# Kernel optimization log

Measured on AMD Instinct MI355X. Metric: run time of the kernel, lower is better.

## Reference

```python
import jax, jax.numpy as jnp
import numpy as np

N_MID = 100000
D = 64
B = 64
S = 256
K = 10
BIG_NEG = -2.0**32 + 1.0


def _din(q, facts, mask, W1, b1, W2, b2, W3, b3):
    # q broadcastable to facts shape; facts [..., T, D]; mask [..., T]
    qb = jnp.broadcast_to(q, facts.shape)
    x = jnp.concatenate([qb, facts, qb - facts, qb * facts], axis=-1)  # [..., T, 4D]
    h = jax.nn.sigmoid(x @ W1 + b1)
    h = jax.nn.sigmoid(h @ W2 + b2)
    s = (h @ W3 + b3)[..., 0]  # [..., T]
    s = jnp.where(mask == 1.0, s, BIG_NEG)
    a = jax.nn.softmax(s, axis=-1)
    return jnp.einsum('...t,...td->...d', a, facts)


def _prelu(x, alpha):
    return jnp.maximum(x, 0.0) + alpha * jnp.minimum(x, 0.0)


def setup_inputs():
    key = jax.random.key(0)
    ks = iter(jax.random.split(key, 48))
    def nrm(shape, scale=0.05):
        return jax.random.normal(next(ks), shape, dtype=jnp.float32) * scale
    inp = {}
    inp['mid'] = jax.random.randint(next(ks), (B,), 0, N_MID)
    inp['click_his'] = jax.random.randint(next(ks), (B, S), 0, N_MID)
    inp['unclick_his'] = jax.random.randint(next(ks), (B, K * S), 0, N_MID)
    inp['click_mask'] = jnp.ones((B, S), jnp.float32)
    inp['unclick_mask'] = jnp.ones((B, K * S), jnp.float32)
    inp['emb'] = nrm((N_MID, D), 0.1)
    for p in ('s', 'c', 'u'):  # search / click / unclick attention MLPs
        inp[p + 'W1'] = nrm((4 * D, 80)); inp[p + 'b1'] = jnp.zeros((80,), jnp.float32)
        inp[p + 'W2'] = nrm((80, 40));    inp[p + 'b2'] = jnp.zeros((40,), jnp.float32)
        inp[p + 'W3'] = nrm((40, 1));     inp[p + 'b3'] = jnp.zeros((1,), jnp.float32)
    F = 3 * D
    inp['bn_g'] = jnp.ones((F,), jnp.float32); inp['bn_b'] = jnp.zeros((F,), jnp.float32)
    inp['bn_m'] = jnp.zeros((F,), jnp.float32); inp['bn_v'] = jnp.ones((F,), jnp.float32)
    inp['fW1'] = nrm((F, 200)); inp['fb1'] = jnp.zeros((200,), jnp.float32); inp['a1'] = 0.25 * jnp.ones((200,), jnp.float32)
    inp['fW2'] = nrm((200, 80)); inp['fb2'] = jnp.zeros((80,), jnp.float32); inp['a2'] = 0.25 * jnp.ones((80,), jnp.float32)
    inp['fW3'] = nrm((80, 2)); inp['fb3'] = jnp.zeros((2,), jnp.float32)
    return inp


def reference(mid, click_his, unclick_his, click_mask, unclick_mask, emb,
              sW1, sb1, sW2, sb2, sW3, sb3,
              cW1, cb1, cW2, cb2, cW3, cb3,
              uW1, ub1, uW2, ub2, uW3, ub3,
              bn_g, bn_b, bn_m, bn_v,
              fW1, fb1, a1, fW2, fb2, a2, fW3, fb3):
    item = emb[mid]                                        # [B, D]
    click = emb[click_his] * click_mask[..., None]         # [B, S, D]
    unclick = emb[unclick_his] * unclick_mask[..., None]   # [B, K*S, D]
    uf = unclick.reshape(B, S, K, D)
    umask = unclick_mask.reshape(B, S, K)
    # din_attention_1: per clicked item, attend over its K unclicked items
    un_att = _din(click[:, :, None, :], uf, umask, sW1, sb1, sW2, sb2, sW3, sb3)  # [B, S, D]
    # denoise: project unclick rep onto click rep (shared component)
    dot = jnp.sum(un_att * click, axis=-1, keepdims=True)
    nrm2 = jnp.sum(click * click, axis=-1, keepdims=True) + 1e-12  # ||target||^2
    shared = dot * click / nrm2
    att1 = _din(item[:, None, :], click + shared, click_mask, cW1, cb1, cW2, cb2, cW3, cb3)  # [B, D]
    att2 = _din(item[:, None, :], un_att, click_mask, uW1, ub1, uW2, ub2, uW3, ub3)          # [B, D]
    x = jnp.concatenate([item, att1, att2], axis=-1)  # [B, 3D]
    x = (x - bn_m) / jnp.sqrt(bn_v + 1e-3) * bn_g + bn_b  # inference batchnorm
    x = _prelu(x @ fW1 + fb1, a1)
    x = _prelu(x @ fW2 + fb2, a2)
    logits = x @ fW3 + fb3
    return jax.nn.softmax(logits, axis=-1) + 1e-8
```

## Files before the change

kernel.cpp:

```cpp
#include <hip/hip_runtime.h>
#include <hip/hip_bf16.h>
#include <math.h>

#define BB 64
#define SS 256
#define KK 10
#define DD 64
#define FF 192
#define FH1 200
#define FH2 80
#define BIG_NEG_F (-4294967295.0f)

#define XSTR 200
#define H1STR 104

#define W1ELTS (80 * XSTR)
#define W2ELTS (48 * H1STR)
#define WREG   (W1ELTS + W2ELTS)

typedef __bf16 bfrag __attribute__((ext_vector_type(8)));
typedef float f32x4 __attribute__((ext_vector_type(4)));

__device__ __forceinline__ float sigm_(float x) { return 1.0f / (1.0f + __expf(-x)); }

__global__ __launch_bounds__(256) void k_prep(
    const float* __restrict__ sW1, const float* __restrict__ sW2,
    const float* __restrict__ cW1, const float* __restrict__ cW2,
    const float* __restrict__ uW1, const float* __restrict__ uW2,
    __bf16* __restrict__ Wt)
{
    const int p = blockIdx.x, g = blockIdx.y;
    const float* W1 = (p == 0) ? sW1 : (p == 1) ? cW1 : uW1;
    const float* W2 = (p == 0) ? sW2 : (p == 1) ? cW2 : uW2;
    __bf16* o1 = Wt + p * WREG;
    __bf16* o2 = o1 + W1ELTS;
    for (int e = g * 256 + threadIdx.x; e < W1ELTS; e += 2560) {
        const int n = e / XSTR, k = e % XSTR;
        float v = 0.0f;
        if (k < 64)       v = W1[k * 80 + n] + W1[(128 + k) * 80 + n];
        else if (k < 128) { const int kk = k - 64;  v = W1[(64 + kk) * 80 + n] - W1[(128 + kk) * 80 + n]; }
        else if (k < 192) { const int kk = k - 128; v = W1[(192 + kk) * 80 + n]; }
        o1[e] = (__bf16)v;
    }
    for (int e = g * 256 + threadIdx.x; e < W2ELTS; e += 2560) {
        const int n = e / H1STR, k = e % H1STR;
        o2[e] = (__bf16)((n < 40 && k < 80) ? W2[k * 40 + n] : 0.0f);
    }
}

__device__ __forceinline__ void mlp_core(
    const float* qv, const float* fv,
    const __bf16* __restrict__ sW1, __bf16* __restrict__ sH1w,
    const bfrag* wb2, const float* b1v, const float* b2v, const float* w3v,
    int quad, int l15, float* score)
{
    bfrag af[6];
    #pragma unroll
    for (int j = 0; j < 8; ++j) {
        af[0][j] = (__bf16)qv[j];
        af[1][j] = (__bf16)qv[8 + j];
        af[2][j] = (__bf16)fv[j];
        af[3][j] = (__bf16)fv[8 + j];
        af[4][j] = (__bf16)(qv[j] * fv[j]);
        af[5][j] = (__bf16)(qv[8 + j] * fv[8 + j]);
    }

    f32x4 acc[5];
    #pragma unroll
    for (int nt = 0; nt < 5; ++nt) acc[nt] = (f32x4){0.f, 0.f, 0.f, 0.f};
    {
        const __bf16* wbase = sW1 + l15 * XSTR + quad * 8;
        #pragma unroll
        for (int nt = 0; nt < 5; ++nt) {
            const __bf16* wp = wbase + nt * 16 * XSTR;
            #pragma unroll
            for (int kc = 0; kc < 6; ++kc)
                acc[nt] = __builtin_amdgcn_mfma_f32_16x16x32_bf16(
                    af[kc], *(const bfrag*)(wp + kc * 32), acc[nt], 0, 0, 0);
        }
    }

    #pragma unroll
    for (int nt = 0; nt < 5; ++nt) {
        #pragma unroll
        for (int rg = 0; rg < 4; ++rg)
            sH1w[(quad * 4 + rg) * H1STR + nt * 16 + l15] =
                (__bf16)sigm_(acc[nt][rg] + b1v[nt]);
    }
    #pragma unroll
    for (int rg = 0; rg < 4; ++rg)
        sH1w[(quad * 4 + rg) * H1STR + 80 + l15] = (__bf16)0.0f;

    bfrag af2[3];
    {
        const __bf16* hrow = sH1w + l15 * H1STR + quad * 8;
        #pragma unroll
        for (int kc = 0; kc < 3; ++kc) af2[kc] = *(const bfrag*)(hrow + kc * 32);
    }
    f32x4 acc2[3];
    #pragma unroll
    for (int nt = 0; nt < 3; ++nt) acc2[nt] = (f32x4){0.f, 0.f, 0.f, 0.f};
    #pragma unroll
    for (int nt = 0; nt < 3; ++nt)
        #pragma unroll
        for (int kc = 0; kc < 3; ++kc)
            acc2[nt] = __builtin_amdgcn_mfma_f32_16x16x32_bf16(
                af2[kc], wb2[nt * 3 + kc], acc2[nt], 0, 0, 0);

    float part[4] = {0.f, 0.f, 0.f, 0.f};
    #pragma unroll
    for (int nt = 0; nt < 3; ++nt) {
        #pragma unroll
        for (int rg = 0; rg < 4; ++rg)
            part[rg] += sigm_(acc2[nt][rg] + b2v[nt]) * w3v[nt];
    }
    #pragma unroll
    for (int off = 1; off < 16; off <<= 1) {
        #pragma unroll
        for (int rg = 0; rg < 4; ++rg)
            part[rg] += __shfl_xor(part[rg], off, 64);
    }
    #pragma unroll
    for (int rg = 0; rg < 4; ++rg) score[rg] = part[rg];
}

__global__ __launch_bounds__(320) void k_din0(
    const int* __restrict__ click_his, const int* __restrict__ unclick_his,
    const float* __restrict__ click_mask, const float* __restrict__ unclick_mask,
    const float* __restrict__ emb, const __bf16* __restrict__ Wt,
    const float* __restrict__ b1, const float* __restrict__ b2,
    const float* __restrict__ W3, const float* __restrict__ b3,
    float* __restrict__ unatt, float* __restrict__ coef)
{
    __shared__ __align__(16) __bf16 sW1[80 * XSTR];
    __shared__ __align__(16) __bf16 sH1[5 * 16 * H1STR];
    __shared__ float ssc[80];

    const int t = threadIdx.x;
    const int wave = t >> 6, lane = t & 63;
    const int quad = lane >> 4, l15 = lane & 15;

    {
        const uint4* s1 = (const uint4*)Wt;
        uint4* d1 = (uint4*)sW1;
        for (int e = t; e < W1ELTS / 8; e += 320) d1[e] = s1[e];
    }

    bfrag wb2[9];
    float b1v[5], b2v[3], w3v[3];
    {
        const __bf16* w2g = Wt + W1ELTS;
        #pragma unroll
        for (int nt = 0; nt < 3; ++nt)
            #pragma unroll
            for (int kc = 0; kc < 3; ++kc)
                wb2[nt * 3 + kc] = *(const bfrag*)(w2g + (nt * 16 + l15) * H1STR + kc * 32 + quad * 8);
        #pragma unroll
        for (int nt = 0; nt < 5; ++nt) b1v[nt] = b1[nt * 16 + l15];
        #pragma unroll
        for (int nt = 0; nt < 3; ++nt) {
            const int n = nt * 16 + l15;
            b2v[nt] = (n < 40) ? b2[n] : 0.0f;
            w3v[nt] = (n < 40) ? W3[n] : 0.0f;
        }
    }
    const float b3v = b3[0];

    const int row = 16 * wave + l15;
    const int m   = blockIdx.x * 80 + row;
    const int bs  = blockIdx.x * 8 + row / 10;
    float qv[16], fv[16];
    {
        const float* qp = emb + (size_t)click_his[bs] * DD;
        const float* fp = emb + (size_t)unclick_his[m] * DD;
        const float qs = click_mask[bs], fs = unclick_mask[m];
        const int c = quad * 8;
        *(float4*)(qv + 0)  = *(const float4*)(qp + c);
        *(float4*)(qv + 4)  = *(const float4*)(qp + c + 4);
        *(float4*)(qv + 8)  = *(const float4*)(qp + 32 + c);
        *(float4*)(qv + 12) = *(const float4*)(qp + 32 + c + 4);
        *(float4*)(fv + 0)  = *(const float4*)(fp + c);
        *(float4*)(fv + 4)  = *(const float4*)(fp + c + 4);
        *(float4*)(fv + 8)  = *(const float4*)(fp + 32 + c);
        *(float4*)(fv + 12) = *(const float4*)(fp + 32 + c + 4);
        #pragma unroll
        for (int i = 0; i < 16; ++i) { qv[i] *= qs; fv[i] *= fs; }
    }
    __syncthreads();

    float score[4];
    mlp_core(qv, fv, sW1, sH1 + wave * 16 * H1STR, wb2, b1v, b2v, w3v, quad, l15, score);

    if (l15 == 0) {
        #pragma unroll
        for (int rg = 0; rg < 4; ++rg) {
            const int r2 = 16 * wave + quad * 4 + rg;
            const int m2 = blockIdx.x * 80 + r2;
            ssc[r2] = (unclick_mask[m2] == 1.0f) ? (score[rg] + b3v) : BIG_NEG_F;
        }
    }
    __syncthreads();

    for (int j = wave; j < 8; j += 5) {
        const int bsj = blockIdx.x * 8 + j;
        float a[KK];
        float mx = -INFINITY;
        #pragma unroll
        for (int k = 0; k < KK; ++k) { a[k] = ssc[j * KK + k]; mx = fmaxf(mx, a[k]); }
        float sum = 0.0f;
        #pragma unroll
        for (int k = 0; k < KK; ++k) { a[k] = __expf(a[k] - mx); sum += a[k]; }
        const float inv = 1.0f / sum;
        float acc3 = 0.0f;
        #pragma unroll
        for (int k = 0; k < KK; ++k) {
            const int off = bsj * KK + k;
            acc3 += a[k] * (emb[(size_t)unclick_his[off] * DD + lane] * unclick_mask[off]);
        }
        acc3 *= inv;
        unatt[(size_t)bsj * DD + lane] = acc3;
        const float qv2 = emb[(size_t)click_his[bsj] * DD + lane] * click_mask[bsj];
        float dp = acc3 * qv2, nq = qv2 * qv2;
        #pragma unroll
        for (int o = 32; o > 0; o >>= 1) {
            dp += __shfl_down(dp, o, 64);
            nq += __shfl_down(nq, o, 64);
        }
        if (lane == 0) coef[bsj] = 1.0f + dp / (nq + 1e-12f);
    }
}

__global__ __launch_bounds__(256) void k_din12(
    const int* __restrict__ mid, const int* __restrict__ click_his,
    const float* __restrict__ click_mask,
    const float* __restrict__ emb, const float* __restrict__ unatt,
    const float* __restrict__ coef, const __bf16* __restrict__ Wt,
    const float* __restrict__ cb1, const float* __restrict__ cb2,
    const float* __restrict__ cW3, const float* __restrict__ cb3,
    const float* __restrict__ ub1, const float* __restrict__ ub2,
    const float* __restrict__ uW3, const float* __restrict__ ub3,
    float* __restrict__ scores_c, float* __restrict__ scores_u)
{
    __shared__ __align__(16) __bf16 sW1[80 * XSTR];
    __shared__ __align__(16) __bf16 sH1[4 * 16 * H1STR];

    const int t = threadIdx.x;
    const int mode = blockIdx.y;
    const int wave = t >> 6, lane = t & 63;
    const int quad = lane >> 4, l15 = lane & 15;

    const float* b1 = mode ? ub1 : cb1;
    const float* b2 = mode ? ub2 : cb2;
    const float* W3 = mode ? uW3 : cW3;
    const float* b3 = mode ? ub3 : cb3;
    const __bf16* wreg = Wt + (mode + 1) * WREG;

    {
        const uint4* s1 = (const uint4*)wreg;
        uint4* d1 = (uint4*)sW1;
        for (int e = t; e < W1ELTS / 8; e += 256) d1[e] = s1[e];
    }

    bfrag wb2[9];
    float b1v[5], b2v[3], w3v[3];
    {
        const __bf16* w2g = wreg + W1ELTS;
        #pragma unroll
        for (int nt = 0; nt < 3; ++nt)
            #pragma unroll
            for (int kc = 0; kc < 3; ++kc)
                wb2[nt * 3 + kc] = *(const bfrag*)(w2g + (nt * 16 + l15) * H1STR + kc * 32 + quad * 8);
        #pragma unroll
        for (int nt = 0; nt < 5; ++nt) b1v[nt] = b1[nt * 16 + l15];
        #pragma unroll
        for (int nt = 0; nt < 3; ++nt) {
            const int n = nt * 16 + l15;
            b2v[nt] = (n < 40) ? b2[n] : 0.0f;
            w3v[nt] = (n < 40) ? W3[n] : 0.0f;
        }
    }
    const float b3v = b3[0];

    const int row = 16 * wave + l15;
    const int m   = blockIdx.x * 64 + row;
    const int b   = m >> 8;
    float qv[16], fv[16];
    {
        const float* qp = emb + (size_t)mid[b] * DD;
        const float* fp; float fs;
        if (mode == 0) { fp = emb + (size_t)click_his[m] * DD; fs = click_mask[m] * coef[m]; }
        else           { fp = unatt + (size_t)m * DD; fs = 1.0f; }
        const int c = quad * 8;
        *(float4*)(qv + 0)  = *(const float4*)(qp + c);
        *(float4*)(qv + 4)  = *(const float4*)(qp + c + 4);
        *(float4*)(qv + 8)  = *(const float4*)(qp + 32 + c);
        *(float4*)(qv + 12) = *(const float4*)(qp + 32 + c + 4);
        *(float4*)(fv + 0)  = *(const float4*)(fp + c);
        *(float4*)(fv + 4)  = *(const float4*)(fp + c + 4);
        *(float4*)(fv + 8)  = *(const float4*)(fp + 32 + c);
        *(float4*)(fv + 12) = *(const float4*)(fp + 32 + c + 4);
        #pragma unroll
        for (int i = 0; i < 16; ++i) fv[i] *= fs;
    }
    __syncthreads();

    float score[4];
    mlp_core(qv, fv, sW1, sH1 + wave * 16 * H1STR, wb2, b1v, b2v, w3v, quad, l15, score);

    if (l15 == 0) {
        float* dst = mode ? scores_u : scores_c;
        #pragma unroll
        for (int rg = 0; rg < 4; ++rg) {
            const int m2 = blockIdx.x * 64 + 16 * wave + quad * 4 + rg;
            dst[m2] = (click_mask[m2] == 1.0f) ? (score[rg] + b3v) : BIG_NEG_F;
        }
    }
}

__global__ __launch_bounds__(256) void k_tail(
    const int* __restrict__ mid, const int* __restrict__ click_his,
    const float* __restrict__ click_mask,
    const float* __restrict__ emb, const float* __restrict__ unatt,
    const float* __restrict__ coef,
    const float* __restrict__ scores_c, const float* __restrict__ scores_u,
    const float* __restrict__ bn_g, const float* __restrict__ bn_b,
    const float* __restrict__ bn_m, const float* __restrict__ bn_v,
    const float* __restrict__ fW1, const float* __restrict__ fb1, const float* __restrict__ a1,
    const float* __restrict__ fW2, const float* __restrict__ fb2, const float* __restrict__ a2,
    const float* __restrict__ fW3, const float* __restrict__ fb3,
    float* __restrict__ out)
{
    const int b = blockIdx.x, t = threadIdx.x;
    const int lane = t & 63, wv = t >> 6;

    __shared__ float x[FF];
    __shared__ float sa[SS];
    __shared__ float red[8];
    __shared__ float part[4][DD];
    __shared__ float h1[FH1];
    __shared__ float h2[FH2];

    if (t < DD) x[t] = emb[(size_t)mid[b] * DD + t];

    for (int ty = 0; ty < 2; ++ty) {
        const float sc = (ty ? scores_u : scores_c)[b * SS + t];
        float m = sc;
        #pragma unroll
        for (int o = 32; o > 0; o >>= 1) m = fmaxf(m, __shfl_down(m, o, 64));
        if (lane == 0) red[wv] = m;
        __syncthreads();
        m = fmaxf(fmaxf(red[0], red[1]), fmaxf(red[2], red[3]));
        const float e = __expf(sc - m);
        sa[t] = e;
        float s = e;
        #pragma unroll
        for (int o = 32; o > 0; o >>= 1) s += __shfl_down(s, o, 64);
        if (lane == 0) red[4 + wv] = s;
        __syncthreads();
        const float inv = 1.0f / (red[4] + red[5] + red[6] + red[7]);

        float acc = 0.0f;
        for (int s2 = wv * 64; s2 < wv * 64 + 64; ++s2) {
            const int bs = b * SS + s2;
            const float fvv = ty ? unatt[(size_t)bs * DD + lane]
                                 : emb[(size_t)click_his[bs] * DD + lane] * click_mask[bs] * coef[bs];
            acc += sa[s2] * inv * fvv;
        }
        part[wv][lane] = acc;
        __syncthreads();
        if (t < DD) x[DD + ty * DD + t] = part[0][t] + part[1][t] + part[2][t] + part[3][t];
        __syncthreads();
    }

    if (t < FF) x[t] = (x[t] - bn_m[t]) * rsqrtf(bn_v[t] + 1e-3f) * bn_g[t] + bn_b[t];
    __syncthreads();
    if (t < FH1) {
        float acc = fb1[t];
        #pragma unroll 4
        for (int i = 0; i < FF; ++i) acc += x[i] * fW1[i * FH1 + t];
        h1[t] = fmaxf(acc, 0.0f) + a1[t] * fminf(acc, 0.0f);
    }
    __syncthreads();
    if (t < FH2) {
        float acc = fb2[t];
        #pragma unroll 4
        for (int i = 0; i < FH1; ++i) acc += h1[i] * fW2[i * FH2 + t];
        h2[t] = fmaxf(acc, 0.0f) + a2[t] * fminf(acc, 0.0f);
    }
    __syncthreads();
    if (t == 0) {
        float l0 = fb3[0], l1 = fb3[1];
        for (int i = 0; i < FH2; ++i) {
            l0 += h2[i] * fW3[i * 2 + 0];
            l1 += h2[i] * fW3[i * 2 + 1];
        }
        const float mx = fmaxf(l0, l1);
        const float e0 = __expf(l0 - mx), e1 = __expf(l1 - mx);
        const float inv = 1.0f / (e0 + e1);
        out[b * 2 + 0] = e0 * inv + 1e-8f;
        out[b * 2 + 1] = e1 * inv + 1e-8f;
    }
}

extern "C" void kernel_launch(void* const* d_in, const int* in_sizes, int n_in,
                              void* d_out, int out_size, void* d_ws, size_t ws_size,
                              hipStream_t stream) {
    const int*   mid          = (const int*)d_in[0];
    const int*   click_his    = (const int*)d_in[1];
    const int*   unclick_his  = (const int*)d_in[2];
    const float* click_mask   = (const float*)d_in[3];
    const float* unclick_mask = (const float*)d_in[4];
    const float* emb          = (const float*)d_in[5];
    const float* sW1 = (const float*)d_in[6];  const float* sb1 = (const float*)d_in[7];
    const float* sW2 = (const float*)d_in[8];  const float* sb2 = (const float*)d_in[9];
    const float* sW3 = (const float*)d_in[10]; const float* sb3 = (const float*)d_in[11];
    const float* cW1 = (const float*)d_in[12]; const float* cb1 = (const float*)d_in[13];
    const float* cW2 = (const float*)d_in[14]; const float* cb2 = (const float*)d_in[15];
    const float* cW3 = (const float*)d_in[16]; const float* cb3 = (const float*)d_in[17];
    const float* uW1 = (const float*)d_in[18]; const float* ub1 = (const float*)d_in[19];
    const float* uW2 = (const float*)d_in[20]; const float* ub2 = (const float*)d_in[21];
    const float* uW3 = (const float*)d_in[22]; const float* ub3 = (const float*)d_in[23];
    const float* bn_g = (const float*)d_in[24]; const float* bn_b = (const float*)d_in[25];
    const float* bn_m = (const float*)d_in[26]; const float* bn_v = (const float*)d_in[27];
    const float* fW1 = (const float*)d_in[28]; const float* fb1 = (const float*)d_in[29];
    const float* a1  = (const float*)d_in[30];
    const float* fW2 = (const float*)d_in[31]; const float* fb2 = (const float*)d_in[32];
    const float* a2  = (const float*)d_in[33];
    const float* fW3 = (const float*)d_in[34]; const float* fb3 = (const float*)d_in[35];

    float* out = (float*)d_out;

    char* w = (char*)d_ws;
    __bf16* Wt      = (__bf16*)(w + 0);
    float* scores_c = (float*)(w + 125952);
    float* scores_u = (float*)(w + 191488);
    float* coef     = (float*)(w + 257024);
    float* unatt    = (float*)(w + 322560);

    hipLaunchKernelGGL(k_prep, dim3(3, 10), dim3(256), 0, stream,
        sW1, sW2, cW1, cW2, uW1, uW2, Wt);

    hipLaunchKernelGGL(k_din0, dim3(2048), dim3(320), 0, stream,
        click_his, unclick_his, click_mask, unclick_mask, emb, Wt,
        sb1, sb2, sW3, sb3, unatt, coef);

    hipLaunchKernelGGL(k_din12, dim3(256, 2), dim3(256), 0, stream,
        mid, click_his, click_mask, emb, unatt, coef, Wt,
        cb1, cb2, cW3, cb3, ub1, ub2, uW3, ub3, scores_c, scores_u);

    hipLaunchKernelGGL(k_tail, dim3(BB), dim3(256), 0, stream,
        mid, click_his, click_mask, emb, unatt, coef, scores_c, scores_u,
        bn_g, bn_b, bn_m, bn_v, fW1, fb1, a1, fW2, fb2, a2, fW3, fb3, out);
}
```

Baseline: 235.6 us.

## Prefetch unclick gathers, split din12 into smaller blocks, parallelize tail kernel

In k_din0, the per-row unclick and click embedding gathers used by the softmax-weighted sum are issued before the MLP, so their latency overlaps the MFMA work instead of stalling afterward. k_din12 moves to 128-thread blocks covering 32 rows, which doubles the grid, but each block now copies the full W1 weight matrix into shared memory for fewer rows. k_tail grows to 1024 threads: both attention types run at once across 16 waves, and the FC layers are split-K with partial sums reduced in shared memory. The extra register arrays in k_din0 and the larger tail block may reduce occupancy.

```diff
diff --git a/kernel.cpp b/kernel.cpp
--- a/kernel.cpp
+++ b/kernel.cpp
@@ -186,6 +186,21 @@
         #pragma unroll
         for (int i = 0; i < 16; ++i) { qv[i] *= qs; fv[i] *= fs; }
     }
+
+    float fpre[2][KK], qpre[2];
+    #pragma unroll
+    for (int jj = 0; jj < 2; ++jj) {
+        const int j = wave + 5 * jj;
+        if (j < 8) {
+            const int bsj = blockIdx.x * 8 + j;
+            #pragma unroll
+            for (int k = 0; k < KK; ++k) {
+                const int off = bsj * KK + k;
+                fpre[jj][k] = emb[(size_t)unclick_his[off] * DD + lane] * unclick_mask[off];
+            }
+            qpre[jj] = emb[(size_t)click_his[bsj] * DD + lane] * click_mask[bsj];
+        }
+    }
     __syncthreads();
 
     float score[4];
@@ -201,7 +216,10 @@
     }
     __syncthreads();
 
-    for (int j = wave; j < 8; j += 5) {
+    #pragma unroll
+    for (int jj = 0; jj < 2; ++jj) {
+        const int j = wave + 5 * jj;
+        if (j >= 8) continue;
         const int bsj = blockIdx.x * 8 + j;
         float a[KK];
         float mx = -INFINITY;
@@ -213,13 +231,10 @@
         const float inv = 1.0f / sum;
         float acc3 = 0.0f;
         #pragma unroll
-        for (int k = 0; k < KK; ++k) {
-            const int off = bsj * KK + k;
-            acc3 += a[k] * (emb[(size_t)unclick_his[off] * DD + lane] * unclick_mask[off]);
-        }
+        for (int k = 0; k < KK; ++k) acc3 += a[k] * fpre[jj][k];
         acc3 *= inv;
         unatt[(size_t)bsj * DD + lane] = acc3;
-        const float qv2 = emb[(size_t)click_his[bsj] * DD + lane] * click_mask[bsj];
+        const float qv2 = qpre[jj];
         float dp = acc3 * qv2, nq = qv2 * qv2;
         #pragma unroll
         for (int o = 32; o > 0; o >>= 1) {
@@ -230,7 +245,7 @@
     }
 }
 
-__global__ __launch_bounds__(256) void k_din12(
+__global__ __launch_bounds__(128) void k_din12(
     const int* __restrict__ mid, const int* __restrict__ click_his,
     const float* __restrict__ click_mask,
     const float* __restrict__ emb, const float* __restrict__ unatt,
@@ -242,7 +257,7 @@
     float* __restrict__ scores_c, float* __restrict__ scores_u)
 {
     __shared__ __align__(16) __bf16 sW1[80 * XSTR];
-    __shared__ __align__(16) __bf16 sH1[4 * 16 * H1STR];
+    __shared__ __align__(16) __bf16 sH1[2 * 16 * H1STR];
 
     const int t = threadIdx.x;
     const int mode = blockIdx.y;
@@ -258,7 +273,7 @@
     {
         const uint4* s1 = (const uint4*)wreg;
         uint4* d1 = (uint4*)sW1;
-        for (int e = t; e < W1ELTS / 8; e += 256) d1[e] = s1[e];
+        for (int e = t; e < W1ELTS / 8; e += 128) d1[e] = s1[e];
     }
 
     bfrag wb2[9];
@@ -282,7 +297,7 @@
     const float b3v = b3[0];
 
     const int row = 16 * wave + l15;
-    const int m   = blockIdx.x * 64 + row;
+    const int m   = blockIdx.x * 32 + row;
     const int b   = m >> 8;
     float qv[16], fv[16];
     {
@@ -311,13 +326,13 @@
         float* dst = mode ? scores_u : scores_c;
         #pragma unroll
         for (int rg = 0; rg < 4; ++rg) {
-            const int m2 = blockIdx.x * 64 + 16 * wave + quad * 4 + rg;
+            const int m2 = blockIdx.x * 32 + 16 * wave + quad * 4 + rg;
             dst[m2] = (click_mask[m2] == 1.0f) ? (score[rg] + b3v) : BIG_NEG_F;
         }
     }
 }
 
-__global__ __launch_bounds__(256) void k_tail(
+__global__ __launch_bounds__(1024) void k_tail(
     const int* __restrict__ mid, const int* __restrict__ click_his,
     const float* __restrict__ click_mask,
     const float* __restrict__ emb, const float* __restrict__ unatt,
@@ -331,74 +346,116 @@
     float* __restrict__ out)
 {
     const int b = blockIdx.x, t = threadIdx.x;
-    const int lane = t & 63, wv = t >> 6;
-
+    const int wave = t >> 6, lane = t & 63;
+    const int ty = wave >> 3, w8 = wave & 7;
+    const int s0 = w8 * 32;
+
+    __shared__ float sa[2][SS];
+    __shared__ float smax[16], ssum[16];
+    __shared__ float part[16][72];
     __shared__ float x[FF];
-    __shared__ float sa[SS];
-    __shared__ float red[8];
-    __shared__ float part[4][DD];
-    __shared__ float h1[FH1];
-    __shared__ float h2[FH2];
+    __shared__ float ph1[4][FH1];
+    __shared__ float h1s[FH1];
+    __shared__ float ph2[8][FH2];
+    __shared__ float h2s[FH2];
+    __shared__ float red2[2];
 
     if (t < DD) x[t] = emb[(size_t)mid[b] * DD + t];
 
-    for (int ty = 0; ty < 2; ++ty) {
-        const float sc = (ty ? scores_u : scores_c)[b * SS + t];
-        float m = sc;
-        #pragma unroll
-        for (int o = 32; o > 0; o >>= 1) m = fmaxf(m, __shfl_down(m, o, 64));
-        if (lane == 0) red[wv] = m;
-        __syncthreads();
-        m = fmaxf(fmaxf(red[0], red[1]), fmaxf(red[2], red[3]));
-        const float e = __expf(sc - m);
-        sa[t] = e;
-        float s = e;
-        #pragma unroll
-        for (int o = 32; o > 0; o >>= 1) s += __shfl_down(s, o, 64);
-        if (lane == 0) red[4 + wv] = s;
-        __syncthreads();
-        const float inv = 1.0f / (red[4] + red[5] + red[6] + red[7]);
-
-        float acc = 0.0f;
-        for (int s2 = wv * 64; s2 < wv * 64 + 64; ++s2) {
-            const int bs = b * SS + s2;
-            const float fvv = ty ? unatt[(size_t)bs * DD + lane]
-                                 : emb[(size_t)click_his[bs] * DD + lane] * click_mask[bs] * coef[bs];
-            acc += sa[s2] * inv * fvv;
-        }
-        part[wv][lane] = acc;
-        __syncthreads();
-        if (t < DD) x[DD + ty * DD + t] = part[0][t] + part[1][t] + part[2][t] + part[3][t];
-        __syncthreads();
-    }
+    const float* scp = ty ? scores_u : scores_c;
+    const float sc = (lane < 32) ? scp[b * SS + s0 + lane] : -INFINITY;
+    float mloc = sc;
+    #pragma unroll
+    for (int o = 32; o > 0; o >>= 1) mloc = fmaxf(mloc, __shfl_xor(mloc, o, 64));
+    if (lane == 0) smax[wave] = mloc;
+    __syncthreads();
+
+    float mt = smax[ty * 8];
+    #pragma unroll
+    for (int i = 1; i < 8; ++i) mt = fmaxf(mt, smax[ty * 8 + i]);
+    const float e = (lane < 32) ? __expf(sc - mt) : 0.0f;
+    if (lane < 32) sa[ty][s0 + lane] = e;
+    float sloc = e;
+    #pragma unroll
+    for (int o = 32; o > 0; o >>= 1) sloc += __shfl_xor(sloc, o, 64);
+    if (lane == 0) ssum[wave] = sloc;
+    __syncthreads();
+
+    float den = 0.0f;
+    #pragma unroll
+    for (int i = 0; i < 8; ++i) den += ssum[ty * 8 + i];
+    const float inv = 1.0f / den;
+
+    float acc = 0.0f;
+    #pragma unroll 8
+    for (int i = 0; i < 32; ++i) {
+        const int s2 = s0 + i;
+        const int bs = b * SS + s2;
+        const float fv = ty ? unatt[(size_t)bs * DD + lane]
+                            : emb[(size_t)click_his[bs] * DD + lane] * click_mask[bs] * coef[bs];
+        acc += sa[ty][s2] * fv;
+    }
+    part[wave][lane] = acc * inv;
+    __syncthreads();
+
+    if (t < 128) {
+        const int tt = t >> 6, d = t & 63;
+        float v = 0.0f;
+        #pragma unroll
+        for (int i = 0; i < 8; ++i) v += part[tt * 8 + i][d];
+        x[DD + tt * DD + d] = v;
+    }
+    __syncthreads();
 
     if (t < FF) x[t] = (x[t] - bn_m[t]) * rsqrtf(bn_v[t] + 1e-3f) * bn_g[t] + bn_b[t];
     __syncthreads();
+
+    if (t < 800) {
+        const int n = t % FH1, c = t / FH1;
+        float p = 0.0f;
+        #pragma unroll 8
+        for (int i = c * 48; i < c * 48 + 48; ++i) p += x[i] * fW1[i * FH1 + n];
+        ph1[c][n] = p;
+    }
+    __syncthreads();
     if (t < FH1) {
-        float acc = fb1[t];
-        #pragma unroll 4
-        for (int i = 0; i < FF; ++i) acc += x[i] * fW1[i * FH1 + t];
-        h1[t] = fmaxf(acc, 0.0f) + a1[t] * fminf(acc, 0.0f);
+        const float a = ph1[0][t] + ph1[1][t] + ph1[2][t] + ph1[3][t] + fb1[t];
+        h1s[t] = fmaxf(a, 0.0f) + a1[t] * fminf(a, 0.0f);
+    }
+    __syncthreads();
+
+    if (t < 640) {
+        const int n = t % FH2, c = t / FH2;
+        float p = 0.0f;
+        #pragma unroll 5
+        for (int i = c * 25; i < c * 25 + 25; ++i) p += h1s[i] * fW2[i * FH2 + n];
+        ph2[c][n] = p;
     }
     __syncthreads();
     if (t < FH2) {
-        float acc = fb2[t];
-        #pragma unroll 4
-        for (int i = 0; i < FH1; ++i) acc += h1[i] * fW2[i * FH2 + t];
-        h2[t] = fmaxf(acc, 0.0f) + a2[t] * fminf(acc, 0.0f);
+        float a = fb2[t];
+        #pragma unroll
+        for (int c = 0; c < 8; ++c) a += ph2[c][t];
+        h2s[t] = fmaxf(a, 0.0f) + a2[t] * fminf(a, 0.0f);
+    }
+    __syncthreads();
+
+    if (t < 128) {
+        const int o = t >> 6;
+        float p = h2s[lane] * fW3[lane * 2 + o];
+        if (lane < 16) p += h2s[64 + lane] * fW3[(64 + lane) * 2 + o];
+        #pragma unroll
+        for (int off = 32; off > 0; off >>= 1) p += __shfl_down(p, off, 64);
+        if (lane == 0) red2[o] = p + fb3[o];
     }
     __syncthreads();
     if (t == 0) {
-        float l0 = fb3[0], l1 = fb3[1];
-        for (int i = 0; i < FH2; ++i) {
-            l0 += h2[i] * fW3[i * 2 + 0];
-            l1 += h2[i] * fW3[i * 2 + 1];
-        }
+        const float l0 = red2[0], l1 = red2[1];
         const float mx = fmaxf(l0, l1);
         const float e0 = __expf(l0 - mx), e1 = __expf(l1 - mx);
-        const float inv = 1.0f / (e0 + e1);
-        out[b * 2 + 0] = e0 * inv + 1e-8f;
-        out[b * 2 + 1] = e1 * inv + 1e-8f;
+        const float invs = 1.0f / (e0 + e1);
+        out[b * 2 + 0] = e0 * invs + 1e-8f;
+        out[b * 2 + 1] = e1 * invs + 1e-8f;
     }
 }
 
@@ -444,11 +501,11 @@
         click_his, unclick_his, click_mask, unclick_mask, emb, Wt,
         sb1, sb2, sW3, sb3, unatt, coef);
 
-    hipLaunchKernelGGL(k_din12, dim3(256, 2), dim3(256), 0, stream,
+    hipLaunchKernelGGL(k_din12, dim3(512, 2), dim3(128), 0, stream,
         mid, click_his, click_mask, emb, unatt, coef, Wt,
         cb1, cb2, cW3, cb3, ub1, ub2, uW3, ub3, scores_c, scores_u);
 
-    hipLaunchKernelGGL(k_tail, dim3(BB), dim3(256), 0, stream,
+    hipLaunchKernelGGL(k_tail, dim3(BB), dim3(1024), 0, stream,
         mid, click_his, click_mask, emb, unatt, coef, scores_c, scores_u,
         bn_g, bn_b, bn_m, bn_v, fW1, fb1, a1, fW2, fb2, a2, fW3, fb3, out);
 }
```

Result: slower. 246.1 us (+4.5%).
